# Optimization experiments

Hardware: AMD Instinct MI355X
Metric: run time of the kernel (lower is better)

Reference implementation:

```python
import jax, jax.numpy as jnp
import numpy as np
from jax import lax

L, B, T = 512, 1024, 48


def setup_inputs() -> dict:
    key = jax.random.key(0)
    k1, k2, k3, k4, k5 = jax.random.split(key, 5)
    emissions = jax.random.normal(k1, (L, B, T), dtype=jnp.float32)
    tags = jax.random.randint(k2, (L, B), 0, T)
    mask = jnp.ones((L, B), dtype=bool)
    start_transitions = jax.random.uniform(k3, (T,), minval=-0.1, maxval=0.1, dtype=jnp.float32)
    end_transitions = jax.random.uniform(k4, (T,), minval=-0.1, maxval=0.1, dtype=jnp.float32)
    transitions = jax.random.uniform(k5, (T, T), minval=-0.1, maxval=0.1, dtype=jnp.float32)
    return {
        'emissions': emissions,
        'tags': tags,
        'mask': mask,
        'start_transitions': start_transitions,
        'end_transitions': end_transitions,
        'transitions': transitions,
    }


def reference(emissions, tags, mask, start_transitions, end_transitions, transitions):
    # emissions: [L, B, T] float; tags: [L, B] int; mask: [L, B] bool (seq-first)
    fm = mask.astype(emissions.dtype)
    seq_len, batch, _ = emissions.shape
    b_idx = jnp.arange(batch)

    # ---- numerator: score of the gold path ----
    # emission score at each step: emissions[i, b, tags[i, b]] -> [L, B]
    em_sc = jnp.take_along_axis(emissions, tags[:, :, None], axis=2)[:, :, 0]
    # transition score between consecutive tags -> [L-1, B]
    trans_sc = transitions[tags[:-1], tags[1:]]
    score = start_transitions[tags[0]] + em_sc[0]
    score = score + jnp.sum((trans_sc + em_sc[1:]) * fm[1:], axis=0)
    seq_ends = mask.astype(jnp.int32).sum(axis=0) - 1  # [B]
    last_tags = tags[seq_ends, b_idx]
    score = score + end_transitions[last_tags]

    # ---- denominator: log partition via forward algorithm (scan) ----
    alpha0 = start_transitions + emissions[0]  # [B, T]

    def step(alpha, xs):
        em, m = xs  # em: [B, T], m: [B]
        # [B, T(prev), T(next)] logsumexp over prev
        next_alpha = jax.nn.logsumexp(
            alpha[:, :, None] + transitions[None, :, :] + em[:, None, :], axis=1)
        alpha = jnp.where(m[:, None], next_alpha, alpha)
        return alpha, None

    alpha, _ = lax.scan(step, alpha0, (emissions[1:], mask[1:]))
    denominator = jax.nn.logsumexp(alpha + end_transitions, axis=1)  # [B]

    llh = score - denominator
    return jnp.mean(llh)  # reduction='mean' (default)
```

## Files before the change

kernel.cpp:

```cpp
#include <hip/hip_runtime.h>

#define LSEQ 512
#define BATCH 1024
#define T 48

typedef float f4 __attribute__((ext_vector_type(4)));
typedef __fp16 h2 __attribute__((ext_vector_type(2)));
typedef __fp16 h4 __attribute__((ext_vector_type(4)));
typedef float f32x4 __attribute__((ext_vector_type(4)));

static __device__ __forceinline__ f32x4 mfma16(h4 a, h4 b, f32x4 c) {
#if defined(__HIP_DEVICE_COMPILE__)
#if __has_builtin(__builtin_amdgcn_mfma_f32_16x16x16f16)
    return __builtin_amdgcn_mfma_f32_16x16x16f16(a, b, c, 0, 0, 0);
#else
    return __builtin_amdgcn_mfma_f32_16x16x16_f16(a, b, c, 0, 0, 0);
#endif
#else
    return c;
#endif
}

static __device__ __forceinline__ h4 pack4(float a, float b, float c, float d) {
    h2 lo = __builtin_amdgcn_cvt_pkrtz(a, b);
    h2 hi = __builtin_amdgcn_cvt_pkrtz(c, d);
    h4 r; r.x = lo.x; r.y = lo.y; r.z = hi.x; r.w = hi.y;
    return r;
}
static __device__ __forceinline__ h4 sel4(bool c, h4 a, h4 b) {
    int2 ai = __builtin_bit_cast(int2, a), bi = __builtin_bit_cast(int2, b);
    int2 r; r.x = c ? ai.x : bi.x; r.y = c ? ai.y : bi.y;
    return __builtin_bit_cast(h4, r);
}
static __device__ __forceinline__ float fast_rcp(float x) {
#if defined(__HIP_DEVICE_COMPILE__) && __has_builtin(__builtin_amdgcn_rcpf)
    return __builtin_amdgcn_rcpf(x);
#else
    return 1.0f / x;
#endif
}

struct Slot { f4 em[3]; int mk; };

__global__ __launch_bounds__(64, 1) void crf_forward(
    const float* __restrict__ emissions,
    const int* __restrict__ mask,
    const float* __restrict__ start_tr,
    const float* __restrict__ end_tr,
    const float* __restrict__ trans,
    float* __restrict__ denom_out)
{
    const int lane  = threadIdx.x;
    const int col   = lane & 15;
    const int g     = lane >> 4;
    const int bbase = blockIdx.x * 16;
    const int b     = bbase + col;

    h4 Af[3][3];
    #pragma unroll
    for (int rb = 0; rb < 3; ++rb)
        #pragma unroll
        for (int kc = 0; kc < 3; ++kc) {
            float e0 = __expf(trans[(16*kc + 4*g + 0)*T + 16*rb + col]);
            float e1 = __expf(trans[(16*kc + 4*g + 1)*T + 16*rb + col]);
            float e2 = __expf(trans[(16*kc + 4*g + 2)*T + 16*rb + col]);
            float e3 = __expf(trans[(16*kc + 4*g + 3)*T + 16*rb + col]);
            Af[rb][kc] = pack4(e0, e1, e2, e3);
        }

    float a[12];
    #pragma unroll
    for (int kc = 0; kc < 3; ++kc) {
        const f4 em0v = *(const f4*)(emissions + (size_t)b * T + 16*kc + 4*g);
        const f4 st4  = *(const f4*)(start_tr + 16*kc + 4*g);
        #pragma unroll
        for (int i = 0; i < 4; ++i) a[4*kc + i] = st4[i] + em0v[i];
    }
    float m = fmaxf(fmaxf(fmaxf(a[0],a[1]), fmaxf(a[2],a[3])),
              fmaxf(fmaxf(fmaxf(a[4],a[5]), fmaxf(a[6],a[7])),
                    fmaxf(fmaxf(a[8],a[9]), fmaxf(a[10],a[11]))));
    m = fmaxf(m, __shfl_xor(m, 16));
    m = fmaxf(m, __shfl_xor(m, 32));
    float C = m;
    h4 Bf[3];
    #pragma unroll
    for (int kc = 0; kc < 3; ++kc)
        Bf[kc] = pack4(__expf(a[4*kc+0]-m), __expf(a[4*kc+1]-m),
                       __expf(a[4*kc+2]-m), __expf(a[4*kc+3]-m));

    auto step = [&](const Slot& S) {
        const f32x4 z = {0.f, 0.f, 0.f, 0.f};
        f32x4 D[3];
        #pragma unroll
        for (int rb = 0; rb < 3; ++rb) {
            D[rb] = mfma16(Af[rb][0], Bf[0], z);
            D[rb] = mfma16(Af[rb][1], Bf[1], D[rb]);
            D[rb] = mfma16(Af[rb][2], Bf[2], D[rb]);
        }
        float y[12];
        #pragma unroll
        for (int kc = 0; kc < 3; ++kc)
            #pragma unroll
            for (int i = 0; i < 4; ++i)
                y[4*kc + i] = __expf(S.em[kc][i]) * D[kc][i];
        float mx = fmaxf(fmaxf(fmaxf(y[0],y[1]), fmaxf(y[2],y[3])),
                   fmaxf(fmaxf(fmaxf(y[4],y[5]), fmaxf(y[6],y[7])),
                         fmaxf(fmaxf(y[8],y[9]), fmaxf(y[10],y[11]))));
        mx = fmaxf(mx, __shfl_xor(mx, 16));
        mx = fmaxf(mx, __shfl_xor(mx, 32));
        const float rs = fast_rcp(mx);
        const float lg = __logf(mx);
        const bool upd = (S.mk != 0);
        #pragma unroll
        for (int kc = 0; kc < 3; ++kc)
            Bf[kc] = sel4(upd,
                          pack4(y[4*kc+0]*rs, y[4*kc+1]*rs,
                                y[4*kc+2]*rs, y[4*kc+3]*rs),
                          Bf[kc]);
        C = upd ? (C + lg) : C;
    };

    auto load = [&](Slot& S, int t) {
        const size_t off = ((size_t)t * BATCH + b) * T + 4*g;
        S.em[0] = *(const f4*)(emissions + off);
        S.em[1] = *(const f4*)(emissions + off + 16);
        S.em[2] = *(const f4*)(emissions + off + 32);
        S.mk    = mask[t * BATCH + b];
    };
    auto loadc = [&](Slot& S, int t) { load(S, t > LSEQ-1 ? LSEQ-1 : t); };

    Slot S0, S1, S2, S3;
    load(S0, 1); load(S1, 2); load(S2, 3); load(S3, 4);
    for (int t = 1; t <= LSEQ - 4; t += 4) {
        step(S0); loadc(S0, t + 4);
        step(S1); loadc(S1, t + 5);
        step(S2); loadc(S2, t + 6);
        step(S3); loadc(S3, t + 7);
    }
    step(S0); step(S1); step(S2);

    float v = 0.f;
    #pragma unroll
    for (int kc = 0; kc < 3; ++kc) {
        const f4 endv = *(const f4*)(end_tr + 16*kc + 4*g);
        #pragma unroll
        for (int i = 0; i < 4; ++i)
            v += (float)Bf[kc][i] * __expf(endv[i]);
    }
    v += __shfl_xor(v, 16);
    v += __shfl_xor(v, 32);
    if (lane < 16) denom_out[bbase + lane] = C + __logf(v);
}

__global__ __launch_bounds__(256) void crf_score_partial(
    const float* __restrict__ emissions,
    const int* __restrict__ tags,
    const int* __restrict__ mask,
    const float* __restrict__ trans,
    float* __restrict__ part,
    int* __restrict__ cnt,
    int csz)
{
    const int gid = blockIdx.x * blockDim.x + threadIdx.x;
    const int b = gid & (BATCH - 1);
    const int c = gid >> 10;
    const int t0 = c * csz;
    const int t1 = t0 + csz;

    float sc = 0.f;
    int ct = 0;
    const int tstart = (t0 == 0) ? 1 : t0;
    if (t0 == 0) ct += mask[b] ? 1 : 0;

    int tag_prev = tags[(tstart - 1) * BATCH + b];
    for (int t = tstart; t < t1; ++t) {
        const int tag = tags[t * BATCH + b];
        const int mt = mask[t * BATCH + b];
        if (mt) {
            sc += trans[tag_prev * T + tag]
                + emissions[((size_t)t * BATCH + b) * T + tag];
            ct += 1;
        }
        tag_prev = tag;
    }
    part[gid] = sc;
    cnt[gid] = ct;
}

__global__ __launch_bounds__(1024) void crf_combine(
    const float* __restrict__ emissions,
    const int* __restrict__ tags,
    const float* __restrict__ start_tr,
    const float* __restrict__ end_tr,
    const float* __restrict__ part,
    const int* __restrict__ cnt,
    const float* __restrict__ denom,
    float* __restrict__ out,
    int nchunk)
{
    const int b = threadIdx.x;

    const int tag0 = tags[b];
    float sc = start_tr[tag0] + emissions[(size_t)b * T + tag0];
    int ct = 0;
    for (int c = 0; c < nchunk; ++c) {
        sc += part[c * BATCH + b];
        ct += cnt[c * BATCH + b];
    }
    if (ct < 1) ct = 1;
    const int last_tag = tags[(ct - 1) * BATCH + b];
    sc += end_tr[last_tag];

    const float llh = sc - denom[b];

    __shared__ float red[1024];
    red[b] = llh;
    __syncthreads();
    #pragma unroll
    for (int s = 512; s > 0; s >>= 1) {
        if (b < s) red[b] += red[b + s];
        __syncthreads();
    }
    if (b == 0) out[0] = red[0] / (float)BATCH;
}

extern "C" void kernel_launch(void* const* d_in, const int* in_sizes, int n_in,
                              void* d_out, int out_size, void* d_ws, size_t ws_size,
                              hipStream_t stream) {
    const float* emissions        = (const float*)d_in[0];
    const int* tags               = (const int*)d_in[1];
    const int* mask               = (const int*)d_in[2];
    const float* start_tr         = (const float*)d_in[3];
    const float* end_tr           = (const float*)d_in[4];
    const float* trans            = (const float*)d_in[5];
    float* out                    = (float*)d_out;

    const int nchunk = (ws_size >= (size_t)(BATCH * 4 + 32 * BATCH * 8 + 64)) ? 32 : 8;
    const int csz    = LSEQ / nchunk;

    float* denom = (float*)d_ws;
    float* part  = denom + BATCH;
    int*   cnt   = (int*)(part + nchunk * BATCH);

    crf_forward<<<BATCH / 16, 64, 0, stream>>>(emissions, mask, start_tr,
                                               end_tr, trans, denom);
    crf_score_partial<<<nchunk * BATCH / 256, 256, 0, stream>>>(
        emissions, tags, mask, trans, part, cnt, csz);
    crf_combine<<<1, 1024, 0, stream>>>(emissions, tags, start_tr, end_tr,
                                        part, cnt, denom, out, nchunk);
}
```

Measured before the change: 231.6 us.

## Stream emissions through LDS with async global_load_lds ring buffer

Replaces the register-held four-slot prefetch in the CRF forward recurrence with a six-slot LDS ring filled by asynchronous global_load_lds, waited on with explicit vmcnt counts and scheduling barriers. The exp of the next step's emissions is computed ahead so it overlaps the MFMA and reduction chain of the current step. The intent is to hide global memory latency on the serial recurrence and free VGPRs. The loop now rounds past the sequence end and masks the extra steps out, and it depends on hand-counted vmcnt values staying correct.

```diff
diff --git a/kernel.cpp b/kernel.cpp
--- a/kernel.cpp
+++ b/kernel.cpp
@@ -3,6 +3,7 @@
 #define LSEQ 512
 #define BATCH 1024
 #define T 48
+#define SLOTS 6
 
 typedef float f4 __attribute__((ext_vector_type(4)));
 typedef __fp16 h2 __attribute__((ext_vector_type(2)));
@@ -20,6 +21,26 @@
     return c;
 #endif
 }
+static __device__ __forceinline__ void sbar0() {
+#if defined(__HIP_DEVICE_COMPILE__)
+    __builtin_amdgcn_sched_barrier(0);
+#endif
+}
+static __device__ __forceinline__ void gll16(const float* g, float* l) {
+#if defined(__HIP_DEVICE_COMPILE__)
+    __builtin_amdgcn_global_load_lds(
+        (const __attribute__((address_space(1))) unsigned int*)g,
+        (__attribute__((address_space(3))) unsigned int*)l, 16, 0, 0);
+#endif
+}
+static __device__ __forceinline__ void gll4(const int* g, int* l) {
+#if defined(__HIP_DEVICE_COMPILE__)
+    __builtin_amdgcn_global_load_lds(
+        (const __attribute__((address_space(1))) unsigned int*)g,
+        (__attribute__((address_space(3))) unsigned int*)l, 4, 0, 0);
+#endif
+}
+#define WAITV(N) do { asm volatile("s_waitcnt vmcnt(" #N ")" ::: "memory"); sbar0(); } while (0)
 
 static __device__ __forceinline__ h4 pack4(float a, float b, float c, float d) {
     h2 lo = __builtin_amdgcn_cvt_pkrtz(a, b);
@@ -39,8 +60,6 @@
     return 1.0f / x;
 #endif
 }
-
-struct Slot { f4 em[3]; int mk; };
 
 __global__ __launch_bounds__(64, 1) void crf_forward(
     const float* __restrict__ emissions,
@@ -50,6 +69,9 @@
     const float* __restrict__ trans,
     float* __restrict__ denom_out)
 {
+    __shared__ __align__(16) float em_lds[SLOTS][3][64][4];
+    __shared__ int mk_lds[SLOTS][64];
+
     const int lane  = threadIdx.x;
     const int col   = lane & 15;
     const int g     = lane >> 4;
@@ -88,7 +110,44 @@
         Bf[kc] = pack4(__expf(a[4*kc+0]-m), __expf(a[4*kc+1]-m),
                        __expf(a[4*kc+2]-m), __expf(a[4*kc+3]-m));
 
-    auto step = [&](const Slot& S) {
+    asm volatile("s_waitcnt vmcnt(0)" ::: "memory");
+    sbar0();
+
+    auto issue_slot = [&](int s, int t) {
+        const int tl = t > LSEQ-1 ? LSEQ-1 : t;
+        const float* gp = emissions + ((size_t)tl * BATCH + b) * T + 4*g;
+        gll16(gp,      &em_lds[s][0][0][0]);
+        gll16(gp + 16, &em_lds[s][1][0][0]);
+        gll16(gp + 32, &em_lds[s][2][0][0]);
+        gll4(mask + tl * BATCH + b, &mk_lds[s][0]);
+    };
+
+    issue_slot(0, 1); issue_slot(1, 2); issue_slot(2, 3);
+    issue_slot(3, 4); issue_slot(4, 5); issue_slot(5, 6);
+    WAITV(20);
+    f4 pexpc[3]; int mkc;
+    {
+        #pragma unroll
+        for (int kc = 0; kc < 3; ++kc) {
+            const f4 v = *(const f4*)&em_lds[0][kc][lane][0];
+            #pragma unroll
+            for (int i = 0; i < 4; ++i) pexpc[kc][i] = __expf(v[i]);
+        }
+        mkc = mk_lds[0][lane];
+    }
+
+    auto body = [&](int t, int s_reuse, int s_next) {
+        issue_slot(s_reuse, t + 6);
+        WAITV(20);
+        f4 pn[3];
+        #pragma unroll
+        for (int kc = 0; kc < 3; ++kc) {
+            const f4 v = *(const f4*)&em_lds[s_next][kc][lane][0];
+            #pragma unroll
+            for (int i = 0; i < 4; ++i) pn[kc][i] = __expf(v[i]);
+        }
+        const int mkn = mk_lds[s_next][lane];
+
         const f32x4 z = {0.f, 0.f, 0.f, 0.f};
         f32x4 D[3];
         #pragma unroll
@@ -102,7 +161,7 @@
         for (int kc = 0; kc < 3; ++kc)
             #pragma unroll
             for (int i = 0; i < 4; ++i)
-                y[4*kc + i] = __expf(S.em[kc][i]) * D[kc][i];
+                y[4*kc + i] = pexpc[kc][i] * D[kc][i];
         float mx = fmaxf(fmaxf(fmaxf(y[0],y[1]), fmaxf(y[2],y[3])),
                    fmaxf(fmaxf(fmaxf(y[4],y[5]), fmaxf(y[6],y[7])),
                          fmaxf(fmaxf(y[8],y[9]), fmaxf(y[10],y[11]))));
@@ -110,7 +169,7 @@
         mx = fmaxf(mx, __shfl_xor(mx, 32));
         const float rs = fast_rcp(mx);
         const float lg = __logf(mx);
-        const bool upd = (S.mk != 0);
+        const bool upd = (mkc != 0) && (t <= LSEQ - 1);
         #pragma unroll
         for (int kc = 0; kc < 3; ++kc)
             Bf[kc] = sel4(upd,
@@ -118,26 +177,17 @@
                                 y[4*kc+2]*rs, y[4*kc+3]*rs),
                           Bf[kc]);
         C = upd ? (C + lg) : C;
+        pexpc[0] = pn[0]; pexpc[1] = pn[1]; pexpc[2] = pn[2]; mkc = mkn;
     };
 
-    auto load = [&](Slot& S, int t) {
-        const size_t off = ((size_t)t * BATCH + b) * T + 4*g;
-        S.em[0] = *(const f4*)(emissions + off);
-        S.em[1] = *(const f4*)(emissions + off + 16);
-        S.em[2] = *(const f4*)(emissions + off + 32);
-        S.mk    = mask[t * BATCH + b];
-    };
-    auto loadc = [&](Slot& S, int t) { load(S, t > LSEQ-1 ? LSEQ-1 : t); };
-
-    Slot S0, S1, S2, S3;
-    load(S0, 1); load(S1, 2); load(S2, 3); load(S3, 4);
-    for (int t = 1; t <= LSEQ - 4; t += 4) {
-        step(S0); loadc(S0, t + 4);
-        step(S1); loadc(S1, t + 5);
-        step(S2); loadc(S2, t + 6);
-        step(S3); loadc(S3, t + 7);
-    }
-    step(S0); step(S1); step(S2);
+    for (int t0 = 1; t0 <= LSEQ - 1; t0 += 6) {
+        body(t0 + 0, 0, 1);
+        body(t0 + 1, 1, 2);
+        body(t0 + 2, 2, 3);
+        body(t0 + 3, 3, 4);
+        body(t0 + 4, 4, 5);
+        body(t0 + 5, 5, 0);
+    }
 
     float v = 0.f;
     #pragma unroll
```

Result: faster. 226.8 us (-2.1%).

## Deepen emission prefetch and compute next-step exponentials ahead of the MFMA chain

Applied to the files above, without the earlier changes.

The serial forward-recursion loop now keeps six slots of emissions and mask in flight instead of four. It also computes the exponentials of the next step's emissions one step ahead, in ping-pong buffers, so they are no longer on the dependent MFMA -> max -> normalize chain. Scheduling barriers stop the compiler from regrouping the loads and exps. In exchange the loop runs a few extra guarded (masked-off) steps at the tail, and register pressure rises from the extra slots.

```diff
diff --git a/kernel.cpp b/kernel.cpp
--- a/kernel.cpp
+++ b/kernel.cpp
@@ -20,7 +20,11 @@
     return c;
 #endif
 }
-
+static __device__ __forceinline__ void sbar0() {
+#if defined(__HIP_DEVICE_COMPILE__)
+    __builtin_amdgcn_sched_barrier(0);
+#endif
+}
 static __device__ __forceinline__ h4 pack4(float a, float b, float c, float d) {
     h2 lo = __builtin_amdgcn_cvt_pkrtz(a, b);
     h2 hi = __builtin_amdgcn_cvt_pkrtz(c, d);
@@ -40,7 +44,7 @@
 #endif
 }
 
-struct Slot { f4 em[3]; int mk; };
+struct Slot { f4 em0, em1, em2; int mk; };
 
 __global__ __launch_bounds__(64, 1) void crf_forward(
     const float* __restrict__ emissions,
@@ -88,7 +92,41 @@
         Bf[kc] = pack4(__expf(a[4*kc+0]-m), __expf(a[4*kc+1]-m),
                        __expf(a[4*kc+2]-m), __expf(a[4*kc+3]-m));
 
-    auto step = [&](const Slot& S) {
+    Slot S0, S1, S2, S3, S4, S5;
+    auto issue = [&](Slot& S, int t) {
+        const int tl = t > LSEQ-1 ? LSEQ-1 : t;
+        const float* p = emissions + ((size_t)tl * BATCH + b) * T + 4*g;
+        S.em0 = *(const f4*)p;
+        S.em1 = *(const f4*)(p + 16);
+        S.em2 = *(const f4*)(p + 32);
+        S.mk  = mask[tl * BATCH + b];
+    };
+
+    issue(S0, 1); issue(S1, 2); issue(S2, 3);
+    issue(S3, 4); issue(S4, 5); issue(S5, 6);
+    sbar0();
+
+    f4 pexpA[3], pexpB[3];  int mkA_, mkB_;
+    #pragma unroll
+    for (int i = 0; i < 4; ++i) {
+        pexpA[0][i] = __expf(S0.em0[i]);
+        pexpA[1][i] = __expf(S0.em1[i]);
+        pexpA[2][i] = __expf(S0.em2[i]);
+    }
+    mkA_ = S0.mk;
+
+    auto body = [&](int t, Slot& Sload, Slot& Snext,
+                    f4* pc, int& mc, f4* pn, int& mn) {
+        issue(Sload, t + 6);
+        sbar0();
+        #pragma unroll
+        for (int i = 0; i < 4; ++i) {
+            pn[0][i] = __expf(Snext.em0[i]);
+            pn[1][i] = __expf(Snext.em1[i]);
+            pn[2][i] = __expf(Snext.em2[i]);
+        }
+        mn = Snext.mk;
+
         const f32x4 z = {0.f, 0.f, 0.f, 0.f};
         f32x4 D[3];
         #pragma unroll
@@ -102,7 +140,7 @@
         for (int kc = 0; kc < 3; ++kc)
             #pragma unroll
             for (int i = 0; i < 4; ++i)
-                y[4*kc + i] = __expf(S.em[kc][i]) * D[kc][i];
+                y[4*kc + i] = pc[kc][i] * D[kc][i];
         float mx = fmaxf(fmaxf(fmaxf(y[0],y[1]), fmaxf(y[2],y[3])),
                    fmaxf(fmaxf(fmaxf(y[4],y[5]), fmaxf(y[6],y[7])),
                          fmaxf(fmaxf(y[8],y[9]), fmaxf(y[10],y[11]))));
@@ -110,7 +148,7 @@
         mx = fmaxf(mx, __shfl_xor(mx, 32));
         const float rs = fast_rcp(mx);
         const float lg = __logf(mx);
-        const bool upd = (S.mk != 0);
+        const bool upd = (mc != 0) && (t <= LSEQ - 1);
         #pragma unroll
         for (int kc = 0; kc < 3; ++kc)
             Bf[kc] = sel4(upd,
@@ -120,24 +158,14 @@
         C = upd ? (C + lg) : C;
     };
 
-    auto load = [&](Slot& S, int t) {
-        const size_t off = ((size_t)t * BATCH + b) * T + 4*g;
-        S.em[0] = *(const f4*)(emissions + off);
-        S.em[1] = *(const f4*)(emissions + off + 16);
-        S.em[2] = *(const f4*)(emissions + off + 32);
-        S.mk    = mask[t * BATCH + b];
-    };
-    auto loadc = [&](Slot& S, int t) { load(S, t > LSEQ-1 ? LSEQ-1 : t); };
-
-    Slot S0, S1, S2, S3;
-    load(S0, 1); load(S1, 2); load(S2, 3); load(S3, 4);
-    for (int t = 1; t <= LSEQ - 4; t += 4) {
-        step(S0); loadc(S0, t + 4);
-        step(S1); loadc(S1, t + 5);
-        step(S2); loadc(S2, t + 6);
-        step(S3); loadc(S3, t + 7);
-    }
-    step(S0); step(S1); step(S2);
+    for (int t0 = 1; t0 <= LSEQ - 1; t0 += 6) {
+        body(t0 + 0, S0, S1, pexpA, mkA_, pexpB, mkB_);
+        body(t0 + 1, S1, S2, pexpB, mkB_, pexpA, mkA_);
+        body(t0 + 2, S2, S3, pexpA, mkA_, pexpB, mkB_);
+        body(t0 + 3, S3, S4, pexpB, mkB_, pexpA, mkA_);
+        body(t0 + 4, S4, S5, pexpA, mkA_, pexpB, mkB_);
+        body(t0 + 5, S5, S0, pexpB, mkB_, pexpA, mkA_);
+    }
 
     float v = 0.f;
     #pragma unroll
```

After: 204.1 us. 1.13x faster.
